# Performance work log

Measured on AMD Instinct MI355X. Metric: run time of the kernel, lower is better.

## Reference

```python
import jax, jax.numpy as jnp
import numpy as np

B, N, F_IN, K, OUT = 64, 512, 6, 8, 3
SLOPE = 0.01  # torch LeakyReLU default negative_slope


def lrelu(x):
    return jnp.where(x >= 0, x, SLOPE * x)


def edge_mlp(e, w1, b1, w2, b2):
    # Linear -> LeakyReLU -> Linear -> LeakyReLU (EdgeConvMLP / mlp1)
    return lrelu(lrelu(e @ w1 + b1) @ w2 + b2)


def dyn_edge_conv(x, w1, b1, w2, b2):
    # x: [B, N, F]. kNN in feature space within each graph (self included,
    # matching torch_cluster.knn used by PyG DynamicEdgeConv).
    x2 = jnp.sum(x * x, -1)                                   # [B, N]
    d = x2[:, :, None] + x2[:, None, :] - 2.0 * jnp.einsum('bnf,bmf->bnm', x, x)
    idx = jax.lax.top_k(-d, K)[1]                              # [B, N, K]
    xj = jax.vmap(lambda xb, ib: xb[ib])(x, idx)               # [B, N, K, F]
    xi = jnp.broadcast_to(x[:, :, None, :], xj.shape)
    e = jnp.concatenate([xi, xj - xi], -1)                     # [B, N, K, 2F]
    h = edge_mlp(e, w1, b1, w2, b2)                            # [B, N, K, 256]
    return h.max(axis=2)                                       # max aggregation


def _lin(key, din, dout):
    kw, kb = jax.random.split(key)
    s = 1.0 / np.sqrt(din)
    w = jax.random.uniform(kw, (din, dout), jnp.float32, -s, s)
    b = jax.random.uniform(kb, (dout,), jnp.float32, -s, s)
    return w, b


def setup_inputs() -> dict:
    key = jax.random.key(0)
    ks = jax.random.split(key, 20)
    inp = {}
    inp['x'] = jax.random.normal(ks[0], (B * N, F_IN), jnp.float32)
    inp['edge_index'] = jax.random.randint(ks[1], (2, B * N * K), 0, B * N, jnp.int64)  # unused
    inp['batch'] = jnp.repeat(jnp.arange(B, dtype=jnp.int64), N)
    dims = [(2 * F_IN, 336, 256), (512, 336, 256), (512, 336, 256), (512, 336, 256)]
    for i, (din, dh, do) in enumerate(dims):
        w1, b1 = _lin(ks[2 + 2 * i], din, dh)
        w2, b2 = _lin(ks[3 + 2 * i], dh, do)
        inp[f'c{i+1}_w1'], inp[f'c{i+1}_b1'] = w1, b1
        inp[f'c{i+1}_w2'], inp[f'c{i+1}_b2'] = w2, b2
    inp['m1_w1'], inp['m1_b1'] = _lin(ks[10], 256 * 4 + F_IN, 336)
    inp['m1_w2'], inp['m1_b2'] = _lin(ks[11], 336, 256)
    inp['m2_w1'], inp['m2_b1'] = _lin(ks[12], 256, 128)
    inp['m2_w2'], inp['m2_b2'] = _lin(ks[13], 128, OUT)
    return inp


def reference(x, edge_index, batch,
              c1_w1, c1_b1, c1_w2, c1_b2,
              c2_w1, c2_b1, c2_w2, c2_b2,
              c3_w1, c3_b1, c3_w2, c3_b2,
              c4_w1, c4_b1, c4_w2, c4_b2,
              m1_w1, m1_b1, m1_w2, m1_b2,
              m2_w1, m2_b1, m2_w2, m2_b2):
    # edge_index is unused: DynamicEdgeConv rebuilds the kNN graph each layer.
    # Equal-sized graphs: reshape instead of segment ops (batch = repeat(arange(B), N)).
    xb = x.reshape(B, N, F_IN)
    x1 = dyn_edge_conv(xb, c1_w1, c1_b1, c1_w2, c1_b2)
    x2 = dyn_edge_conv(x1, c2_w1, c2_b1, c2_w2, c2_b2)
    x3 = dyn_edge_conv(x2, c3_w1, c3_b1, c3_w2, c3_b2)
    x4 = dyn_edge_conv(x3, c4_w1, c4_b1, c4_w2, c4_b2)
    h = jnp.concatenate([xb, x1, x2, x3, x4], -1)   # [B, N, 1030]
    h = edge_mlp(h, m1_w1, m1_b1, m1_w2, m1_b2)     # [B, N, 256]
    g = h.mean(axis=1)                              # global_mean_pool -> [B, 256]
    return lrelu(g @ m2_w1 + m2_b1) @ m2_w2 + m2_b2  # [B, OUT]
```

## Files before the change

### kernel.cpp

```cpp
#include <hip/hip_runtime.h>
#include <hip/hip_bf16.h>


#define DEVFN __device__ __forceinline__
DEVFN float lrelu(float v) { return v >= 0.f ? v : 0.01f * v; }

using bf16x8 = __attribute__((ext_vector_type(8))) short;
using f32x4  = __attribute__((ext_vector_type(4))) float;

template<int N> struct IC { static constexpr int value = N; };

DEVFN unsigned short f2bf(float v) {
    __hip_bfloat16 h = __float2bfloat16(v);
    return *(unsigned short*)&h;
}
DEVFN float bf2f(unsigned short u) {
    return __uint_as_float((unsigned)u << 16);
}

struct PDesc { const float* src; unsigned short* dst; int Kt, NT, N, mode, p0, p1, Ksrc; };
struct PTable { PDesc d[13]; };

__global__ __launch_bounds__(256) void pack_kernel(PTable tb) {
    PDesc d = tb.d[blockIdx.y];
    int i = blockIdx.x * 256 + threadIdx.x;
    int tot = d.Kt * d.NT * 512;
    if (i >= tot) return;
    int j = i & 7, lane = (i >> 3) & 63;
    int tile = i >> 9;
    int nt = tile % d.NT, kt = tile / d.NT;
    int k = kt * 32 + ((lane >> 4) << 3) + j;
    int n = nt * 16 + (lane & 15);
    float v = 0.f;
    if (d.mode == 0) {
        if (k < d.Ksrc) v = d.src[(size_t)k * d.N + n];
    } else if (d.mode == 1) {
        if (k < d.p1) v = d.src[(size_t)k * d.N + n] - d.src[(size_t)(k + d.p1) * d.N + n];
        else if (k >= d.p0 && k < d.p0 + d.p1) v = d.src[(size_t)(k - d.p0 + d.p1) * d.N + n];
    } else if (d.mode == 2) {
        if (k < 6) v = d.src[(size_t)k * d.N + n];
        else if (k >= 32 && k < 1056) v = d.src[(size_t)(k - 26) * d.N + n];
    } else {
        v = d.src[(size_t)(k + d.p0) * d.N + n];
    }
    d.dst[i] = f2bf(v);
}

__global__ __launch_bounds__(256) void xbprep_kernel(const float* __restrict__ xb,
                                                     unsigned short* __restrict__ xbbf,
                                                     unsigned short* __restrict__ xcat) {
    int p = blockIdx.x * 256 + threadIdx.x;
    if (p >= 32768) return;
    unsigned short r[16];
    #pragma unroll
    for (int c = 0; c < 6; ++c) r[c] = f2bf(xb[p * 6 + c]);
    #pragma unroll
    for (int c = 6; c < 16; ++c) r[c] = 0;
    #pragma unroll
    for (int c = 0; c < 16; ++c) xbbf[p * 16 + c] = r[c];
    unsigned short* xc = xcat + (size_t)p * 1056;
    #pragma unroll
    for (int c = 0; c < 16; ++c) xc[c] = r[c];
    #pragma unroll
    for (int c = 16; c < 32; ++c) xc[c] = 0;
}

template<int F>
__global__ __launch_bounds__(256) void norms_kernel(const float* __restrict__ f,
                                                    float* __restrict__ nrm) {
    int p = blockIdx.x * 256 + threadIdx.x;
    if (p >= 64 * 512) return;
    const float* r = f + (size_t)p * F;
    float s = 0.f;
    #pragma unroll
    for (int i = 0; i < F; ++i) s += r[i] * r[i];
    nrm[p] = s;
}

template<int F>
__global__ __launch_bounds__(256) void knn_kernel(const float* __restrict__ feat,
                                                  const float* __restrict__ nrm,
                                                  int* __restrict__ knn) {
    constexpr int FP = (F == 6) ? 8 : (F + 4);
    __shared__ float Xq[32 * FP];
    __shared__ float Xc[32 * FP];
    __shared__ float qn[32], cn[32];
    __shared__ float dt[32 * 33];
    const int t  = threadIdx.x;
    const int b  = blockIdx.x >> 4;
    const int n0 = (blockIdx.x & 15) << 5;
    const float* fg = feat + (size_t)b * 512 * F;

    for (int i = t; i < 32 * F; i += 256) {
        int r = i / F, c = i - r * F;
        Xq[r * FP + c] = fg[(size_t)(n0 + r) * F + c];
    }
    if (t < 32) qn[t] = nrm[b * 512 + n0 + t];

    float d8[8]; int i8[8];
    #pragma unroll
    for (int k = 0; k < 8; ++k) { d8[k] = 3.4e38f; i8[k] = 0; }

    const int q = t >> 3, cs = t & 7;

    for (int ct = 0; ct < 16; ++ct) {
        const int c0 = ct << 5;
        __syncthreads();
        for (int i = t; i < 32 * F; i += 256) {
            int r = i / F, c = i - r * F;
            Xc[r * FP + c] = fg[(size_t)(c0 + r) * F + c];
        }
        if (t < 32) cn[t] = nrm[b * 512 + c0 + t];
        __syncthreads();

        float acc[4] = {0.f, 0.f, 0.f, 0.f};
        #pragma unroll
        for (int f = 0; f < F; ++f) {
            float qv = Xq[q * FP + f];
            #pragma unroll
            for (int j = 0; j < 4; ++j) acc[j] += qv * Xc[(cs + 8 * j) * FP + f];
        }
        #pragma unroll
        for (int j = 0; j < 4; ++j)
            dt[q * 33 + cs + 8 * j] = qn[q] + cn[cs + 8 * j] - 2.f * acc[j];
        __syncthreads();

        if (t < 32) {
            #pragma unroll 1
            for (int i = 0; i < 32; ++i) {
                float d = dt[t * 33 + i];
                if (d < d8[7]) {
                    d8[7] = d; i8[7] = c0 + i;
                    #pragma unroll
                    for (int s = 7; s >= 1; --s) {
                        if (d8[s] < d8[s - 1]) {
                            float td = d8[s]; d8[s] = d8[s - 1]; d8[s - 1] = td;
                            int   ti = i8[s]; i8[s] = i8[s - 1]; i8[s - 1] = ti;
                        }
                    }
                }
            }
        }
    }
    if (t < 32) {
        #pragma unroll
        for (int k = 0; k < 8; ++k)
            knn[((size_t)b * 512 + n0 + t) * 8 + k] = i8[k];
    }
}

__global__ __launch_bounds__(256, 2)
void knn_mfma(const unsigned short* __restrict__ xfl,
              const float* __restrict__ nrm,
              int* __restrict__ knn) {
    __shared__ unsigned short Qh[64 * 72], Ql[64 * 72], Ch[64 * 72], Cl[64 * 72];
    __shared__ float dt[64 * 66];
    __shared__ float qn[64], cn[64];
    float* mD = dt;
    int*   mI = (int*)(dt + 2048);

    const int t  = threadIdx.x;
    const int l  = t & 63, w = t >> 6;
    const int m16 = l & 15, q4 = l >> 4;
    const int bx = blockIdx.x;
    const int slot = bx >> 3;
    const int b  = (bx & 7) + 8 * (slot >> 3);
    const int qs = (slot & 7) << 6;

    if (t < 64) qn[t] = nrm[b * 512 + qs + t];

    float d8[8]; int i8[8];
    #pragma unroll
    for (int k = 0; k < 8; ++k) { d8[k] = 3.4e38f; i8[k] = 0x7fffffff; }

    const int sr = t >> 2;
    const int sc = (t & 3) << 4;
    const int tq = t & 63, sub = t >> 6;

    for (int cs = 0; cs < 8; ++cs) {
        const int c0 = cs << 6;
        if (t < 64) cn[t] = nrm[b * 512 + c0 + t];

        f32x4 acc[4];
        #pragma unroll
        for (int i = 0; i < 4; ++i) acc[i] = (f32x4){0.f, 0.f, 0.f, 0.f};

        for (int kc = 0; kc < 4; ++kc) {
            const int k0 = kc << 6;
            __syncthreads();
            {
                const unsigned short* qr = xfl + (size_t)(b * 512 + qs + sr) * 512;
                const unsigned short* cr = xfl + (size_t)(b * 512 + c0 + sr) * 512;
                *(uint4*)&Qh[sr * 72 + sc]     = *(const uint4*)(qr + k0 + sc);
                *(uint4*)&Qh[sr * 72 + sc + 8] = *(const uint4*)(qr + k0 + sc + 8);
                *(uint4*)&Ql[sr * 72 + sc]     = *(const uint4*)(qr + 256 + k0 + sc);
                *(uint4*)&Ql[sr * 72 + sc + 8] = *(const uint4*)(qr + 256 + k0 + sc + 8);
                *(uint4*)&Ch[sr * 72 + sc]     = *(const uint4*)(cr + k0 + sc);
                *(uint4*)&Ch[sr * 72 + sc + 8] = *(const uint4*)(cr + k0 + sc + 8);
                *(uint4*)&Cl[sr * 72 + sc]     = *(const uint4*)(cr + 256 + k0 + sc);
                *(uint4*)&Cl[sr * 72 + sc + 8] = *(const uint4*)(cr + 256 + k0 + sc + 8);
            }
            __syncthreads();

            #pragma unroll
            for (int kt = 0; kt < 2; ++kt) {
                const int ko = kt * 32 + q4 * 8;
                bf16x8 ah = *(const bf16x8*)&Qh[(w * 16 + m16) * 72 + ko];
                bf16x8 al = *(const bf16x8*)&Ql[(w * 16 + m16) * 72 + ko];
                #pragma unroll
                for (int nt = 0; nt < 4; ++nt) {
                    bf16x8 bh = *(const bf16x8*)&Ch[(nt * 16 + m16) * 72 + ko];
                    bf16x8 bl = *(const bf16x8*)&Cl[(nt * 16 + m16) * 72 + ko];
                    acc[nt] = __builtin_amdgcn_mfma_f32_16x16x32_bf16(ah, bh, acc[nt], 0, 0, 0);
                    acc[nt] = __builtin_amdgcn_mfma_f32_16x16x32_bf16(ah, bl, acc[nt], 0, 0, 0);
                    acc[nt] = __builtin_amdgcn_mfma_f32_16x16x32_bf16(al, bh, acc[nt], 0, 0, 0);
                }
            }
        }

        #pragma unroll
        for (int nt = 0; nt < 4; ++nt) {
            float cv = cn[nt * 16 + m16];
            #pragma unroll
            for (int rr = 0; rr < 4; ++rr) {
                int qr = w * 16 + q4 * 4 + rr;
                dt[qr * 66 + nt * 16 + m16] = qn[qr] + cv - 2.f * acc[nt][rr];
            }
        }
        __syncthreads();

        {
            const float* drow = &dt[tq * 66 + sub * 16];
            #pragma unroll 1
            for (int j = 0; j < 16; ++j) {
                float d = drow[j];
                if (d < d8[7]) {
                    d8[7] = d; i8[7] = c0 + sub * 16 + j;
                    #pragma unroll
                    for (int s = 7; s >= 1; --s) {
                        if (d8[s] < d8[s - 1]) {
                            float td = d8[s]; d8[s] = d8[s - 1]; d8[s - 1] = td;
                            int   ti = i8[s]; i8[s] = i8[s - 1]; i8[s - 1] = ti;
                        }
                    }
                }
            }
        }
        __syncthreads();
    }

    #pragma unroll
    for (int k = 0; k < 8; ++k) {
        mD[(tq * 4 + sub) * 8 + k] = d8[k];
        mI[(tq * 4 + sub) * 8 + k] = i8[k];
    }
    __syncthreads();
    if (t < 64) {
        int p[4] = {0, 0, 0, 0};
        int outb = (b * 512 + qs + t) * 8;
        #pragma unroll 1
        for (int k = 0; k < 8; ++k) {
            float bd = 3.5e38f; int bi = 0x7fffffff; int bs = 0;
            #pragma unroll
            for (int s = 0; s < 4; ++s) {
                if (p[s] < 8) {
                    float dd = mD[(t * 4 + s) * 8 + p[s]];
                    int   ii = mI[(t * 4 + s) * 8 + p[s]];
                    if (dd < bd || (dd == bd && ii < bi)) { bd = dd; bi = ii; bs = s; }
                }
            }
            knn[outb + k] = bi;
            p[bs]++;
        }
    }
}

__global__ __launch_bounds__(256, 2)
void pgemm_kernel(const unsigned short* __restrict__ xfl,
                  const unsigned short* __restrict__ Wa,
                  const unsigned short* __restrict__ Wb,
                  const float* __restrict__ B1,
                  unsigned short* __restrict__ Pa,
                  unsigned short* __restrict__ Pb) {
    __shared__ unsigned short smem[64 * 344];
    const int t = threadIdx.x;
    const int l = t & 63, w = t >> 6;
    const int q4 = l >> 4, m16 = l & 15;
    const int s1 = w * 6;
    const int bx = blockIdx.x & 511;
    const bool isA = !(blockIdx.x & 512);
    const unsigned short* W1ap = isA ? Wa : Wb;
    unsigned short*       Pp   = isA ? Pa : Pb;
    const int slot = bx >> 3;
    const int r0 = ((bx & 7) + 8 * (slot >> 3)) * 512 + (slot & 7) * 64;

    {
        const int r = t >> 2;
        const unsigned short* srow = xfl + (size_t)(r0 + r) * 512;
        #pragma unroll
        for (int s = 0; s < 8; ++s) {
            int c16 = (t & 3) + (s << 2);
            *(uint4*)&smem[r * 264 + c16 * 8] = *(const uint4*)(srow + c16 * 8);
        }
    }
    __syncthreads();

    f32x4 acc[4][6];
    #pragma unroll
    for (int mt = 0; mt < 4; ++mt)
        #pragma unroll
        for (int n = 0; n < 6; ++n) acc[mt][n] = (f32x4){0.f, 0.f, 0.f, 0.f};

    auto run = [&](auto c1c) {
        constexpr int C1 = decltype(c1c)::value;
        bf16x8 bcur[C1];
        {
            const unsigned short* bp = W1ap + ((size_t)s1 * 64 + l) * 8;
            #pragma unroll
            for (int n = 0; n < C1; ++n) bcur[n] = *(const bf16x8*)(bp + n * 512);
        }
        #pragma unroll 1
        for (int kt = 0; kt < 8; ++kt) {
            bf16x8 bnext[C1];
            if (kt + 1 < 8) {
                const unsigned short* bp = W1ap + ((size_t)((kt + 1) * 21 + s1) * 64 + l) * 8;
                #pragma unroll
                for (int n = 0; n < C1; ++n) bnext[n] = *(const bf16x8*)(bp + n * 512);
            }
            bf16x8 af[4];
            #pragma unroll
            for (int mt = 0; mt < 4; ++mt)
                af[mt] = *(const bf16x8*)&smem[(mt * 16 + m16) * 264 + q4 * 8 + kt * 32];
            #pragma unroll
            for (int n = 0; n < C1; ++n)
                #pragma unroll
                for (int mt = 0; mt < 4; ++mt)
                    acc[mt][n] = __builtin_amdgcn_mfma_f32_16x16x32_bf16(af[mt], bcur[n], acc[mt][n], 0, 0, 0);
            #pragma unroll
            for (int n = 0; n < C1; ++n) bcur[n] = bnext[n];
        }
    };
    if (w < 3) run(IC<6>{});
    else       run(IC<3>{});

    __syncthreads();
    {
        const int c1 = (w < 3) ? 6 : 3;
        for (int n = 0; n < c1; ++n) {
            int col = (s1 + n) * 16 + m16;
            float bias = isA ? B1[col] : 0.f;
            #pragma unroll
            for (int mt = 0; mt < 4; ++mt)
                #pragma unroll
                for (int r = 0; r < 4; ++r)
                    smem[(mt * 16 + q4 * 4 + r) * 344 + col] = f2bf(acc[mt][n][r] + bias);
        }
    }
    __syncthreads();
    {
        uint4* dst = (uint4*)(Pp + (size_t)r0 * 336);
        const uint4* src = (const uint4*)smem;
        #pragma unroll 1
        for (int i = t; i < 2688; i += 256)
            dst[i] = src[(i / 42) * 43 + (i % 42)];
    }
}

template<int MODE>
__global__ __launch_bounds__(256, 3)
void mfma_mlp(const unsigned short* __restrict__ featbf,
              const int* __restrict__ knn,
              const unsigned short* __restrict__ W1p, const float* __restrict__ B1,
              const unsigned short* __restrict__ W2p, const float* __restrict__ B2,
              const unsigned short* __restrict__ Pp,
              const unsigned short* __restrict__ Pbp,
              float* __restrict__ outf,
              unsigned short* __restrict__ xcat, int sliceoff,
              unsigned short* __restrict__ xfl, float* __restrict__ nrm) {
    constexpr int NCHUNK  = (MODE == 2) ? 3 : 1;
    constexpr int KTPC    = (MODE == 1) ? 1 : 11;
    constexpr int ASTRIDE = (MODE == 1) ? 40 : 360;
    constexpr int MT      = (MODE == 2) ? 2 : 4;
    constexpr int ROWS    = MT * 16;
    constexpr int EXTRA   = (MODE == 1) ? 1024 : (MODE == 3) ? 2048 : 0;

    __shared__ unsigned short smem[ROWS * 360 + EXTRA];
    __shared__ int rowi[64];
    __shared__ int rowj[64];
    __shared__ float nparts[8][4];

    const int t = threadIdx.x;
    const int l = t & 63, w = t >> 6;
    const int q4 = l >> 4, m16 = l & 15;
    const int s1 = w * 6;
    const int s2 = w * 4;

    const int bx = blockIdx.x;
    int p0;
    if constexpr (MODE != 2) {
        int slot = bx >> 3;
        int g = (bx & 7) + 8 * (slot >> 6);
        p0 = g * 512 + (slot & 63) * 8;
    } else {
        int slot = bx >> 3;
        int g = (bx & 7) + 8 * (slot >> 4);
        p0 = g * 512 + (slot & 15) * 32;
    }

    if (MODE != 2 && t < 64) {
        int pt = p0 + (t >> 3);
        rowi[t] = pt;
        rowj[t] = (pt & ~511) + knn[pt * 8 + (t & 7)];
    }

    if constexpr (MODE == 3) {
        __syncthreads();
        const int row = t >> 2;
        const int u0  = t & 3;
        const unsigned short* va = Pp  + (size_t)rowi[row] * 336;
        const unsigned short* vb = Pbp + (size_t)rowj[row] * 336;
        uint4 A[11], Bv[11];
        #pragma unroll
        for (int k = 0; k < 11; ++k) {
            int u = u0 + 4 * k;
            if (u < 42) {
                A[k]  = *(const uint4*)(va + u * 8);
                Bv[k] = *(const uint4*)(vb + u * 8);
            }
        }
        #pragma unroll
        for (int k = 0; k < 11; ++k) {
            int u = u0 + 4 * k;
            if (u < 42) {
                const unsigned short* sa = (const unsigned short*)&A[k];
                const unsigned short* sb = (const unsigned short*)&Bv[k];
                uint4 ov;
                unsigned short* o = (unsigned short*)&ov;
                #pragma unroll
                for (int j = 0; j < 8; ++j)
                    o[j] = f2bf(lrelu(bf2f(sa[j]) + bf2f(sb[j])));
                *(uint4*)&smem[row * 360 + u * 8] = ov;
            }
        }
    } else {
        f32x4 acc1[MT][6];
        #pragma unroll
        for (int mt = 0; mt < MT; ++mt)
            #pragma unroll
            for (int n = 0; n < 6; ++n) acc1[mt][n] = (f32x4){0.f, 0.f, 0.f, 0.f};

        auto g1 = [&](auto c1c, int ktbase) {
            constexpr int C1 = decltype(c1c)::value;
            bf16x8 bcur[C1];
            {
                const unsigned short* bp =
                    W1p + ((size_t)(ktbase * 21 + s1) * 64 + l) * 8;
                #pragma unroll
                for (int n = 0; n < C1; ++n) bcur[n] = *(const bf16x8*)(bp + n * 512);
            }
            #pragma unroll 1
            for (int kt = 0; kt < KTPC; ++kt) {
                bf16x8 bnext[C1];
                if (kt + 1 < KTPC) {
                    const unsigned short* bp =
                        W1p + ((size_t)((ktbase + kt + 1) * 21 + s1) * 64 + l) * 8;
                    #pragma unroll
                    for (int n = 0; n < C1; ++n) bnext[n] = *(const bf16x8*)(bp + n * 512);
                }
                bf16x8 af[MT];
                #pragma unroll
                for (int mt = 0; mt < MT; ++mt)
                    af[mt] = *(const bf16x8*)&smem[(mt * 16 + m16) * ASTRIDE + q4 * 8 + kt * 32];
                #pragma unroll
                for (int n = 0; n < C1; ++n)
                    #pragma unroll
                    for (int mt = 0; mt < MT; ++mt)
                        acc1[mt][n] = __builtin_amdgcn_mfma_f32_16x16x32_bf16(af[mt], bcur[n], acc1[mt][n], 0, 0, 0);
                #pragma unroll
                for (int n = 0; n < C1; ++n) bcur[n] = bnext[n];
            }
        };

        for (int kc = 0; kc < NCHUNK; ++kc) {
            __syncthreads();
            if constexpr (MODE == 1) {
                const int r = t >> 2, c16 = t & 3;
                const unsigned short* s2p =
                    featbf + (size_t)(c16 < 2 ? rowi[r] : rowj[r]) * 16 + (c16 & 1) * 8;
                *(uint4*)&smem[r * 40 + c16 * 8] = *(const uint4*)s2p;
            } else {
                const int r = t >> 3, tc = t & 7;
                const unsigned short* srow =
                    featbf + (size_t)(p0 + r) * 1056 + kc * 352;
                #pragma unroll
                for (int s = 0; s < 6; ++s) {
                    int c16 = tc + (s << 3);
                    if (c16 < 44)
                        *(uint4*)&smem[r * 360 + c16 * 8] = *(const uint4*)(srow + c16 * 8);
                }
            }
            __syncthreads();

            if (w < 3) g1(IC<6>{}, kc * KTPC);
            else       g1(IC<3>{}, kc * KTPC);
        }
        __syncthreads();

        {
            const int c1 = (w < 3) ? 6 : 3;
            for (int n = 0; n < c1; ++n) {
                int nt = s1 + n;
                float b = B1[nt * 16 + m16];
                #pragma unroll
                for (int mt = 0; mt < MT; ++mt) {
                    #pragma unroll
                    for (int r = 0; r < 4; ++r) {
                        int row = mt * 16 + q4 * 4 + r;
                        float v = acc1[mt][n][r] + b;
                        smem[row * 360 + nt * 16 + m16] = f2bf(lrelu(v));
                    }
                }
            }
        }
    }

    if (t < ROWS) {
        #pragma unroll
        for (int c = 336; c < 352; ++c) smem[t * 360 + c] = 0;
    }
    __syncthreads();

    f32x4 acc2[MT][4];
    #pragma unroll
    for (int mt = 0; mt < MT; ++mt)
        #pragma unroll
        for (int n = 0; n < 4; ++n) acc2[mt][n] = (f32x4){0.f, 0.f, 0.f, 0.f};
    {
        bf16x8 b0[4], b1f[4];
        {
            const unsigned short* bp0 = W2p + ((size_t)s2 * 64 + l) * 8;
            const unsigned short* bp1 = W2p + ((size_t)(16 + s2) * 64 + l) * 8;
            #pragma unroll
            for (int n = 0; n < 4; ++n) {
                b0[n]  = *(const bf16x8*)(bp0 + n * 512);
                b1f[n] = *(const bf16x8*)(bp1 + n * 512);
            }
        }
        #pragma unroll 1
        for (int kt = 0; kt < 11; ++kt) {
            bf16x8 b2[4];
            if (kt + 2 < 11) {
                const unsigned short* bp = W2p + ((size_t)((kt + 2) * 16 + s2) * 64 + l) * 8;
                #pragma unroll
                for (int n = 0; n < 4; ++n) b2[n] = *(const bf16x8*)(bp + n * 512);
            }
            bf16x8 af[MT];
            #pragma unroll
            for (int mt = 0; mt < MT; ++mt)
                af[mt] = *(const bf16x8*)&smem[(mt * 16 + m16) * 360 + q4 * 8 + kt * 32];
            #pragma unroll
            for (int n = 0; n < 4; ++n)
                #pragma unroll
                for (int mt = 0; mt < MT; ++mt)
                    acc2[mt][n] = __builtin_amdgcn_mfma_f32_16x16x32_bf16(af[mt], b0[n], acc2[mt][n], 0, 0, 0);
            #pragma unroll
            for (int n = 0; n < 4; ++n) { b0[n] = b1f[n]; b1f[n] = b2[n]; }
        }
    }

    if constexpr (MODE != 2) {
        __syncthreads();
        unsigned short* sh = smem;
        #pragma unroll
        for (int mt = 0; mt < 4; ++mt) {
            float nsum = 0.f;
            int plocal = mt * 2 + (q4 >> 1);
            #pragma unroll
            for (int n = 0; n < 4; ++n) {
                int nt = s2 + n;
                float b = B2[nt * 16 + m16];
                float mv = -3.4e38f;
                #pragma unroll
                for (int r = 0; r < 4; ++r) mv = fmaxf(mv, lrelu(acc2[mt][n][r] + b));
                mv = fmaxf(mv, __shfl_xor(mv, 16, 64));
                if ((q4 & 1) == 0) {
                    int col = nt * 16 + m16;
                    unsigned short hi = f2bf(mv);
                    float fhi = bf2f(hi);
                    unsigned short lo = f2bf(mv - fhi);
                    float xr = fhi + bf2f(lo);
                    nsum += xr * xr;
                    sh[plocal * 512 + col] = hi;
                    sh[plocal * 512 + 256 + col] = lo;
                }
            }
            #pragma unroll
            for (int o = 1; o < 16; o <<= 1) nsum += __shfl_xor(nsum, o, 64);
            if ((q4 & 1) == 0 && m16 == 0) nparts[plocal][w] = nsum;
        }
        __syncthreads();
        {
            int r = t >> 5, cb = (t & 31) * 16;
            int p = p0 + r;
            uint4 v0 = *(uint4*)&sh[r * 512 + cb];
            uint4 v1 = *(uint4*)&sh[r * 512 + cb + 8];
            *(uint4*)&xfl[(size_t)p * 512 + cb]     = v0;
            *(uint4*)&xfl[(size_t)p * 512 + cb + 8] = v1;
            if (cb < 256) {
                *(uint4*)&xcat[(size_t)p * 1056 + sliceoff + cb]     = v0;
                *(uint4*)&xcat[(size_t)p * 1056 + sliceoff + cb + 8] = v1;
            }
        }
        if (t < 8)
            nrm[p0 + t] =
                nparts[t][0] + nparts[t][1] + nparts[t][2] + nparts[t][3];
    } else {
        #pragma unroll
        for (int mt = 0; mt < MT; ++mt)
            #pragma unroll
            for (int n = 0; n < 4; ++n) {
                int nt = s2 + n;
                float b = B2[nt * 16 + m16];
                int col = nt * 16 + m16;
                #pragma unroll
                for (int r = 0; r < 4; ++r) {
                    int p = p0 + mt * 16 + q4 * 4 + r;
                    outf[(size_t)p * 256 + col] = lrelu(acc2[mt][n][r] + b);
                }
            }
    }
}

__global__ __launch_bounds__(256) void pool_kernel(const float* __restrict__ h,
                                                   float* __restrict__ g) {
    int b = blockIdx.x, t = threadIdx.x;
    const float* hb = h + (size_t)b * 512 * 256;
    float s = 0.f;
    for (int n = 0; n < 512; ++n) s += hb[n * 256 + t];
    g[b * 256 + t] = s * (1.f / 512.f);
}

__global__ __launch_bounds__(128) void head_kernel(const float* __restrict__ g,
                                                   const float* __restrict__ w1,
                                                   const float* __restrict__ b1,
                                                   const float* __restrict__ w2,
                                                   const float* __restrict__ b2,
                                                   float* __restrict__ out) {
    __shared__ float gs[256];
    __shared__ float hid[128];
    int b = blockIdx.x, t = threadIdx.x;
    gs[t] = g[b * 256 + t];
    gs[t + 128] = g[b * 256 + t + 128];
    __syncthreads();
    float s = b1[t];
    for (int c = 0; c < 256; ++c) s += gs[c] * w1[c * 128 + t];
    hid[t] = lrelu(s);
    __syncthreads();
    if (t < 3) {
        float o = b2[t];
        for (int j = 0; j < 128; ++j) o += hid[j] * w2[j * 3 + t];
        out[b * 3 + t] = o;
    }
}

extern "C" void kernel_launch(void* const* d_in, const int* in_sizes, int n_in,
                              void* d_out, int out_size, void* d_ws, size_t ws_size,
                              hipStream_t stream) {
    const float* xb = (const float*)d_in[0];
    const float* c_w1[4] = { (const float*)d_in[3],  (const float*)d_in[7],
                             (const float*)d_in[11], (const float*)d_in[15] };
    const float* c_b1[4] = { (const float*)d_in[4],  (const float*)d_in[8],
                             (const float*)d_in[12], (const float*)d_in[16] };
    const float* c_w2[4] = { (const float*)d_in[5],  (const float*)d_in[9],
                             (const float*)d_in[13], (const float*)d_in[17] };
    const float* c_b2[4] = { (const float*)d_in[6],  (const float*)d_in[10],
                             (const float*)d_in[14], (const float*)d_in[18] };
    const float* m1w1 = (const float*)d_in[19];
    const float* m1b1 = (const float*)d_in[20];
    const float* m1w2 = (const float*)d_in[21];
    const float* m1b2 = (const float*)d_in[22];
    const float* m2w1 = (const float*)d_in[23];
    const float* m2b1 = (const float*)d_in[24];
    const float* m2w2 = (const float*)d_in[25];
    const float* m2b2 = (const float*)d_in[26];

    char* base = (char*)d_ws;
    size_t off = 0;
    auto alloc = [&](size_t bytes) { char* p = base + off; off = (off + bytes + 255) & ~(size_t)255; return p; };
    int*            knn   = (int*)           alloc((size_t)32768 * 8 * 4);
    float*          nrm   = (float*)         alloc((size_t)32768 * 4);
    char*           Preg  =                  alloc((size_t)32768 * 256 * 4);
    unsigned short* Ppb   = (unsigned short*)alloc((size_t)32768 * 336 * 2);
    float*          g     = (float*)         alloc(64 * 256 * 4);
    unsigned short* xcat  = (unsigned short*)alloc((size_t)32768 * 1056 * 2);
    unsigned short* xfl   = (unsigned short*)alloc((size_t)32768 * 512 * 2);
    unsigned short* xbbf  = (unsigned short*)alloc((size_t)32768 * 16 * 2);
    unsigned short* w1p1  = (unsigned short*)alloc((size_t)1  * 21 * 512 * 2);
    unsigned short* w2p1  = (unsigned short*)alloc((size_t)11 * 16 * 512 * 2);
    unsigned short* w1a[3]; unsigned short* w1b[3]; unsigned short* w2p[3];
    for (int i = 0; i < 3; ++i) {
        w1a[i] = (unsigned short*)alloc((size_t)8  * 21 * 512 * 2);
        w1b[i] = (unsigned short*)alloc((size_t)8  * 21 * 512 * 2);
        w2p[i] = (unsigned short*)alloc((size_t)11 * 16 * 512 * 2);
    }
    unsigned short* m1p1  = (unsigned short*)alloc((size_t)33 * 21 * 512 * 2);
    unsigned short* m1p2  = (unsigned short*)alloc((size_t)11 * 16 * 512 * 2);
    unsigned short* Pp = (unsigned short*)Preg;
    float*          hm = (float*)Preg;

    PTable tb;
    tb.d[0] = { c_w1[0], w1p1, 1,  21, 336, 1, 16,  6,   0   };
    tb.d[1] = { c_w2[0], w2p1, 11, 16, 256, 0, 0,   0,   336 };
    for (int i = 0; i < 3; ++i) {
        tb.d[2 + 3 * i] = { c_w1[i + 1], w1a[i], 8,  21, 336, 1, 0,   256, 0   };
        tb.d[3 + 3 * i] = { c_w1[i + 1], w1b[i], 8,  21, 336, 3, 256, 0,   0   };
        tb.d[4 + 3 * i] = { c_w2[i + 1], w2p[i], 11, 16, 256, 0, 0,   0,   336 };
    }
    tb.d[11] = { m1w1, m1p1, 33, 21, 336, 2, 0, 0, 0   };
    tb.d[12] = { m1w2, m1p2, 11, 16, 256, 0, 0, 0, 336 };
    pack_kernel<<<dim3(1386, 13), dim3(256), 0, stream>>>(tb);
    xbprep_kernel<<<128, 256, 0, stream>>>(xb, xbbf, xcat);

    norms_kernel<6><<<128, 256, 0, stream>>>(xb, nrm);
    knn_kernel<6><<<1024, 256, 0, stream>>>(xb, nrm, knn);
    mfma_mlp<1><<<4096, 256, 0, stream>>>(xbbf, knn,
                                          w1p1, c_b1[0], w2p1, c_b2[0], nullptr, nullptr,
                                          nullptr, xcat, 32, xfl, nrm);

    for (int l = 1; l < 4; ++l) {
        int dstslice = 32 + l * 256;
        knn_mfma<<<512, 256, 0, stream>>>(xfl, nrm, knn);
        pgemm_kernel<<<1024, 256, 0, stream>>>(xfl, w1a[l - 1], w1b[l - 1], c_b1[l], Pp, Ppb);
        mfma_mlp<3><<<4096, 256, 0, stream>>>(nullptr, knn,
                                              nullptr, nullptr, w2p[l - 1], c_b2[l], Pp, Ppb,
                                              nullptr, xcat, dstslice, xfl, nrm);
    }

    mfma_mlp<2><<<1024, 256, 0, stream>>>(xcat, nullptr,
                                          m1p1, m1b1, m1p2, m1b2, nullptr, nullptr,
                                          hm, nullptr, 0, nullptr, nullptr);

    pool_kernel<<<64, 256, 0, stream>>>(hm, g);
    head_kernel<<<64, 128, 0, stream>>>(g, m2w1, m2b1, m2w2, m2b2, (float*)d_out);
}
```

Baseline: 1.047 ms.

## Decompose first edge-conv layer via per-point projections and shrink MODE3 tiles

Layer 1 now precomputes per-point first-linear projections in fp32 with a scalar kernel (W_a−W_b applied to x_i, W_b applied to x_j), so the fused MLP can reuse the gather-add path instead of running the MODE1 edge GEMM. The MODE1 path and the xbbf buffer are removed. MODE3 blocks are halved to 4 points (32 edge rows) with twice as many blocks and a higher occupancy bound, which trades weight reuse per block for more parallelism. The first-layer projection is rounded to bf16, which changes numerics slightly.

```diff
diff --git a/kernel.cpp b/kernel.cpp
--- a/kernel.cpp
+++ b/kernel.cpp
@@ -47,7 +47,6 @@
 }
 
 __global__ __launch_bounds__(256) void xbprep_kernel(const float* __restrict__ xb,
-                                                     unsigned short* __restrict__ xbbf,
                                                      unsigned short* __restrict__ xcat) {
     int p = blockIdx.x * 256 + threadIdx.x;
     if (p >= 32768) return;
@@ -56,8 +55,6 @@
     for (int c = 0; c < 6; ++c) r[c] = f2bf(xb[p * 6 + c]);
     #pragma unroll
     for (int c = 6; c < 16; ++c) r[c] = 0;
-    #pragma unroll
-    for (int c = 0; c < 16; ++c) xbbf[p * 16 + c] = r[c];
     unsigned short* xc = xcat + (size_t)p * 1056;
     #pragma unroll
     for (int c = 0; c < 16; ++c) xc[c] = r[c];
@@ -273,6 +270,40 @@
             p[bs]++;
         }
     }
+}
+
+__global__ __launch_bounds__(256)
+void pgemm1_kernel(const float* __restrict__ xb,
+                   const float* __restrict__ W1,
+                   const float* __restrict__ B1,
+                   unsigned short* __restrict__ Pa,
+                   unsigned short* __restrict__ Pb) {
+    int i = blockIdx.x * 256 + threadIdx.x;
+    if (i >= 32768 * 42) return;
+    int p = i / 42, c8 = i - p * 42;
+    int c0 = c8 * 8;
+    float x[6];
+    #pragma unroll
+    for (int k = 0; k < 6; ++k) x[k] = xb[p * 6 + k];
+    float sa[8], sb[8];
+    #pragma unroll
+    for (int j = 0; j < 8; ++j) { sa[j] = B1[c0 + j]; sb[j] = 0.f; }
+    #pragma unroll
+    for (int k = 0; k < 6; ++k) {
+        const float* wra = W1 + (size_t)k * 336 + c0;
+        const float* wrb = W1 + (size_t)(k + 6) * 336 + c0;
+        #pragma unroll
+        for (int j = 0; j < 8; ++j) {
+            float wb = wrb[j];
+            sa[j] += x[k] * (wra[j] - wb);
+            sb[j] += x[k] * wb;
+        }
+    }
+    unsigned short oa[8], ob[8];
+    #pragma unroll
+    for (int j = 0; j < 8; ++j) { oa[j] = f2bf(sa[j]); ob[j] = f2bf(sb[j]); }
+    *(uint4*)&Pa[(size_t)p * 336 + c0] = *(uint4*)oa;
+    *(uint4*)&Pb[(size_t)p * 336 + c0] = *(uint4*)ob;
 }
 
 __global__ __launch_bounds__(256, 2)
@@ -367,7 +398,7 @@
 }
 
 template<int MODE>
-__global__ __launch_bounds__(256, 3)
+__global__ __launch_bounds__(256, MODE == 3 ? 4 : 3)
 void mfma_mlp(const unsigned short* __restrict__ featbf,
               const int* __restrict__ knn,
               const unsigned short* __restrict__ W1p, const float* __restrict__ B1,
@@ -377,17 +408,12 @@
               float* __restrict__ outf,
               unsigned short* __restrict__ xcat, int sliceoff,
               unsigned short* __restrict__ xfl, float* __restrict__ nrm) {
-    constexpr int NCHUNK  = (MODE == 2) ? 3 : 1;
-    constexpr int KTPC    = (MODE == 1) ? 1 : 11;
-    constexpr int ASTRIDE = (MODE == 1) ? 40 : 360;
-    constexpr int MT      = (MODE == 2) ? 2 : 4;
-    constexpr int ROWS    = MT * 16;
-    constexpr int EXTRA   = (MODE == 1) ? 1024 : (MODE == 3) ? 2048 : 0;
-
-    __shared__ unsigned short smem[ROWS * 360 + EXTRA];
-    __shared__ int rowi[64];
-    __shared__ int rowj[64];
-    __shared__ float nparts[8][4];
+    constexpr int ROWS = 32;
+
+    __shared__ unsigned short smem[ROWS * 360];
+    __shared__ int rowi[32];
+    __shared__ int rowj[32];
+    __shared__ float nparts[4][4];
 
     const int t = threadIdx.x;
     const int l = t & 63, w = t >> 6;
@@ -397,40 +423,39 @@
 
     const int bx = blockIdx.x;
     int p0;
-    if constexpr (MODE != 2) {
+    if constexpr (MODE == 3) {
         int slot = bx >> 3;
-        int g = (bx & 7) + 8 * (slot >> 6);
-        p0 = g * 512 + (slot & 63) * 8;
+        int g = (bx & 7) + 8 * (slot >> 7);
+        p0 = g * 512 + (slot & 127) * 4;
     } else {
         int slot = bx >> 3;
         int g = (bx & 7) + 8 * (slot >> 4);
         p0 = g * 512 + (slot & 15) * 32;
     }
 
-    if (MODE != 2 && t < 64) {
-        int pt = p0 + (t >> 3);
-        rowi[t] = pt;
-        rowj[t] = (pt & ~511) + knn[pt * 8 + (t & 7)];
-    }
-
     if constexpr (MODE == 3) {
-        __syncthreads();
-        const int row = t >> 2;
-        const int u0  = t & 3;
+        if (t < 32) {
+            int pt = p0 + (t >> 3);
+            rowi[t] = pt;
+            rowj[t] = (pt & ~511) + knn[pt * 8 + (t & 7)];
+        }
+        __syncthreads();
+        const int row = t >> 3;
+        const int u0  = t & 7;
         const unsigned short* va = Pp  + (size_t)rowi[row] * 336;
         const unsigned short* vb = Pbp + (size_t)rowj[row] * 336;
-        uint4 A[11], Bv[11];
-        #pragma unroll
-        for (int k = 0; k < 11; ++k) {
-            int u = u0 + 4 * k;
+        uint4 A[6], Bv[6];
+        #pragma unroll
+        for (int k = 0; k < 6; ++k) {
+            int u = u0 + 8 * k;
             if (u < 42) {
                 A[k]  = *(const uint4*)(va + u * 8);
                 Bv[k] = *(const uint4*)(vb + u * 8);
             }
         }
         #pragma unroll
-        for (int k = 0; k < 11; ++k) {
-            int u = u0 + 4 * k;
+        for (int k = 0; k < 6; ++k) {
+            int u = u0 + 8 * k;
             if (u < 42) {
                 const unsigned short* sa = (const unsigned short*)&A[k];
                 const unsigned short* sb = (const unsigned short*)&Bv[k];
@@ -443,9 +468,9 @@
             }
         }
     } else {
-        f32x4 acc1[MT][6];
-        #pragma unroll
-        for (int mt = 0; mt < MT; ++mt)
+        f32x4 acc1[2][6];
+        #pragma unroll
+        for (int mt = 0; mt < 2; ++mt)
             #pragma unroll
             for (int n = 0; n < 6; ++n) acc1[mt][n] = (f32x4){0.f, 0.f, 0.f, 0.f};
 
@@ -459,36 +484,31 @@
                 for (int n = 0; n < C1; ++n) bcur[n] = *(const bf16x8*)(bp + n * 512);
             }
             #pragma unroll 1
-            for (int kt = 0; kt < KTPC; ++kt) {
+            for (int kt = 0; kt < 11; ++kt) {
                 bf16x8 bnext[C1];
-                if (kt + 1 < KTPC) {
+                if (kt + 1 < 11) {
                     const unsigned short* bp =
                         W1p + ((size_t)((ktbase + kt + 1) * 21 + s1) * 64 + l) * 8;
                     #pragma unroll
                     for (int n = 0; n < C1; ++n) bnext[n] = *(const bf16x8*)(bp + n * 512);
                 }
-                bf16x8 af[MT];
-                #pragma unroll
-                for (int mt = 0; mt < MT; ++mt)
-                    af[mt] = *(const bf16x8*)&smem[(mt * 16 + m16) * ASTRIDE + q4 * 8 + kt * 32];
+                bf16x8 af[2];
+                #pragma unroll
+                for (int mt = 0; mt < 2; ++mt)
+                    af[mt] = *(const bf16x8*)&smem[(mt * 16 + m16) * 360 + q4 * 8 + kt * 32];
                 #pragma unroll
                 for (int n = 0; n < C1; ++n)
                     #pragma unroll
-                    for (int mt = 0; mt < MT; ++mt)
+                    for (int mt = 0; mt < 2; ++mt)
                         acc1[mt][n] = __builtin_amdgcn_mfma_f32_16x16x32_bf16(af[mt], bcur[n], acc1[mt][n], 0, 0, 0);
                 #pragma unroll
                 for (int n = 0; n < C1; ++n) bcur[n] = bnext[n];
             }
         };
 
-        for (int kc = 0; kc < NCHUNK; ++kc) {
+        for (int kc = 0; kc < 3; ++kc) {
             __syncthreads();
-            if constexpr (MODE == 1) {
-                const int r = t >> 2, c16 = t & 3;
-                const unsigned short* s2p =
-                    featbf + (size_t)(c16 < 2 ? rowi[r] : rowj[r]) * 16 + (c16 & 1) * 8;
-                *(uint4*)&smem[r * 40 + c16 * 8] = *(const uint4*)s2p;
-            } else {
+            {
                 const int r = t >> 3, tc = t & 7;
                 const unsigned short* srow =
                     featbf + (size_t)(p0 + r) * 1056 + kc * 352;
@@ -501,8 +521,8 @@
             }
             __syncthreads();
 
-            if (w < 3) g1(IC<6>{}, kc * KTPC);
-            else       g1(IC<3>{}, kc * KTPC);
+            if (w < 3) g1(IC<6>{}, kc * 11);
+            else       g1(IC<3>{}, kc * 11);
         }
         __syncthreads();
 
@@ -512,7 +532,7 @@
                 int nt = s1 + n;
                 float b = B1[nt * 16 + m16];
                 #pragma unroll
-                for (int mt = 0; mt < MT; ++mt) {
+                for (int mt = 0; mt < 2; ++mt) {
                     #pragma unroll
                     for (int r = 0; r < 4; ++r) {
                         int row = mt * 16 + q4 * 4 + r;
@@ -530,9 +550,9 @@
     }
     __syncthreads();
 
-    f32x4 acc2[MT][4];
-    #pragma unroll
-    for (int mt = 0; mt < MT; ++mt)
+    f32x4 acc2[2][4];
+    #pragma unroll
+    for (int mt = 0; mt < 2; ++mt)
         #pragma unroll
         for (int n = 0; n < 4; ++n) acc2[mt][n] = (f32x4){0.f, 0.f, 0.f, 0.f};
     {
@@ -554,25 +574,25 @@
                 #pragma unroll
                 for (int n = 0; n < 4; ++n) b2[n] = *(const bf16x8*)(bp + n * 512);
             }
-            bf16x8 af[MT];
-            #pragma unroll
-            for (int mt = 0; mt < MT; ++mt)
+            bf16x8 af[2];
+            #pragma unroll
+            for (int mt = 0; mt < 2; ++mt)
                 af[mt] = *(const bf16x8*)&smem[(mt * 16 + m16) * 360 + q4 * 8 + kt * 32];
             #pragma unroll
             for (int n = 0; n < 4; ++n)
                 #pragma unroll
-                for (int mt = 0; mt < MT; ++mt)
+                for (int mt = 0; mt < 2; ++mt)
                     acc2[mt][n] = __builtin_amdgcn_mfma_f32_16x16x32_bf16(af[mt], b0[n], acc2[mt][n], 0, 0, 0);
             #pragma unroll
             for (int n = 0; n < 4; ++n) { b0[n] = b1f[n]; b1f[n] = b2[n]; }
         }
     }
 
-    if constexpr (MODE != 2) {
+    if constexpr (MODE == 3) {
         __syncthreads();
         unsigned short* sh = smem;
         #pragma unroll
-        for (int mt = 0; mt < 4; ++mt) {
+        for (int mt = 0; mt < 2; ++mt) {
             float nsum = 0.f;
             int plocal = mt * 2 + (q4 >> 1);
             #pragma unroll
@@ -600,23 +620,19 @@
         }
         __syncthreads();
         {
-            int r = t >> 5, cb = (t & 31) * 16;
+            int r = t >> 6, cb = (t & 63) * 8;
             int p = p0 + r;
             uint4 v0 = *(uint4*)&sh[r * 512 + cb];
-            uint4 v1 = *(uint4*)&sh[r * 512 + cb + 8];
-            *(uint4*)&xfl[(size_t)p * 512 + cb]     = v0;
-            *(uint4*)&xfl[(size_t)p * 512 + cb + 8] = v1;
-            if (cb < 256) {
-                *(uint4*)&xcat[(size_t)p * 1056 + sliceoff + cb]     = v0;
-                *(uint4*)&xcat[(size_t)p * 1056 + sliceoff + cb + 8] = v1;
-            }
-        }
-        if (t < 8)
+            *(uint4*)&xfl[(size_t)p * 512 + cb] = v0;
+            if (cb < 256)
+                *(uint4*)&xcat[(size_t)p * 1056 + sliceoff + cb] = v0;
+        }
+        if (t < 4)
             nrm[p0 + t] =
                 nparts[t][0] + nparts[t][1] + nparts[t][2] + nparts[t][3];
     } else {
         #pragma unroll
-        for (int mt = 0; mt < MT; ++mt)
+        for (int mt = 0; mt < 2; ++mt)
             #pragma unroll
             for (int n = 0; n < 4; ++n) {
                 int nt = s2 + n;
@@ -694,7 +710,6 @@
     float*          g     = (float*)         alloc(64 * 256 * 4);
     unsigned short* xcat  = (unsigned short*)alloc((size_t)32768 * 1056 * 2);
     unsigned short* xfl   = (unsigned short*)alloc((size_t)32768 * 512 * 2);
-    unsigned short* xbbf  = (unsigned short*)alloc((size_t)32768 * 16 * 2);
     unsigned short* w1p1  = (unsigned short*)alloc((size_t)1  * 21 * 512 * 2);
     unsigned short* w2p1  = (unsigned short*)alloc((size_t)11 * 16 * 512 * 2);
     unsigned short* w1a[3]; unsigned short* w1b[3]; unsigned short* w2p[3];
@@ -719,19 +734,20 @@
     tb.d[11] = { m1w1, m1p1, 33, 21, 336, 2, 0, 0, 0   };
     tb.d[12] = { m1w2, m1p2, 11, 16, 256, 0, 0, 0, 336 };
     pack_kernel<<<dim3(1386, 13), dim3(256), 0, stream>>>(tb);
-    xbprep_kernel<<<128, 256, 0, stream>>>(xb, xbbf, xcat);
+    xbprep_kernel<<<128, 256, 0, stream>>>(xb, xcat);
 
     norms_kernel<6><<<128, 256, 0, stream>>>(xb, nrm);
     knn_kernel<6><<<1024, 256, 0, stream>>>(xb, nrm, knn);
-    mfma_mlp<1><<<4096, 256, 0, stream>>>(xbbf, knn,
-                                          w1p1, c_b1[0], w2p1, c_b2[0], nullptr, nullptr,
+    pgemm1_kernel<<<5376, 256, 0, stream>>>(xb, c_w1[0], c_b1[0], Pp, Ppb);
+    mfma_mlp<3><<<8192, 256, 0, stream>>>(nullptr, knn,
+                                          nullptr, nullptr, w2p1, c_b2[0], Pp, Ppb,
                                           nullptr, xcat, 32, xfl, nrm);
 
     for (int l = 1; l < 4; ++l) {
         int dstslice = 32 + l * 256;
         knn_mfma<<<512, 256, 0, stream>>>(xfl, nrm, knn);
         pgemm_kernel<<<1024, 256, 0, stream>>>(xfl, w1a[l - 1], w1b[l - 1], c_b1[l], Pp, Ppb);
-        mfma_mlp<3><<<4096, 256, 0, stream>>>(nullptr, knn,
+        mfma_mlp<3><<<8192, 256, 0, stream>>>(nullptr, knn,
                                               nullptr, nullptr, w2p[l - 1], c_b2[l], Pp, Ppb,
                                               nullptr, xcat, dstslice, xfl, nrm);
     }
```

Result: faster. 1.010 ms (-3.5%).
